# Performance work log

Measured on AMD Instinct MI355X. Metric: run time of the kernel, lower is better.

Reference implementation:

```python
import jax, jax.numpy as jnp
import numpy as np

N = 50000        # total nodes (disjoint batch of graphs)
E = 800000       # total edges
F_IN = 8         # node feature dim
S = 6            # edge feature dim
H = 20           # ECC kernel-network hidden size (hidden_states)
N_OUT = 20       # ECC output channels (n_out=hidden_states)
G = 32           # GCN channels
D1 = 16          # first dense
N_GRAPHS = 512   # graphs in batch


def setup_inputs() -> dict:
    key = jax.random.key(0)
    ks = jax.random.split(key, 24)
    r = lambda k, sh, s: jax.random.normal(k, sh, dtype=jnp.float32) * s
    return {
        "x": r(ks[0], (N, F_IN), 1.0),
        "e": r(ks[1], (E, S), 1.0),
        "edge_index": jax.random.randint(ks[2], (2, E), 0, N, dtype=jnp.int32),
        "seg": jnp.sort(jax.random.randint(ks[3], (N,), 0, N_GRAPHS, dtype=jnp.int32)),
        # ECC kernel network: S -> H -> H -> F_IN*N_OUT
        "ecc_w1": r(ks[4], (S, H), 0.4), "ecc_b1": jnp.zeros((H,), jnp.float32),
        "ecc_w2": r(ks[5], (H, H), 0.2), "ecc_b2": jnp.zeros((H,), jnp.float32),
        "ecc_w3": r(ks[6], (H, F_IN * N_OUT), 0.2), "ecc_b3": jnp.zeros((F_IN * N_OUT,), jnp.float32),
        "ecc_root": r(ks[7], (F_IN, N_OUT), 0.3), "ecc_b": jnp.zeros((N_OUT,), jnp.float32),
        "gcn1_w": r(ks[8], (N_OUT, G), 0.2), "gcn1_b": jnp.zeros((G,), jnp.float32),
        "gcn2_w": r(ks[9], (G, G), 0.2), "gcn2_b": jnp.zeros((G,), jnp.float32),
        "d1_w": r(ks[10], (G, D1), 0.2), "d1_b": jnp.zeros((D1,), jnp.float32),
        "d2_w": r(ks[11], (D1, 1), 0.2), "d2_b": jnp.zeros((1,), jnp.float32),
    }


def reference(x, e, edge_index, seg,
              ecc_w1, ecc_b1, ecc_w2, ecc_b2, ecc_w3, ecc_b3, ecc_root, ecc_b,
              gcn1_w, gcn1_b, gcn2_w, gcn2_b, d1_w, d1_b, d2_w, d2_b):
    row, col = edge_index[0], edge_index[1]  # message col -> row

    # --- ECCConv: per-edge MLP produces an [F_IN, N_OUT] filter per edge ---
    h = jax.nn.relu(e @ ecc_w1 + ecc_b1)
    h = jax.nn.relu(h @ ecc_w2 + ecc_b2)
    w_edge = (h @ ecc_w3 + ecc_b3).reshape(E, F_IN, N_OUT)   # [E, F_in, F_out]
    msg = jnp.einsum('ef,efo->eo', x[col], w_edge)            # per-edge message
    agg = jax.ops.segment_sum(msg, row, num_segments=N)
    x1 = jax.nn.relu(agg + x @ ecc_root + ecc_b)              # root + bias + relu

    # --- GCN normalization from the edge list (A + I, symmetric norm) ---
    deg = jax.ops.segment_sum(jnp.ones((E,), x.dtype), row, num_segments=N) + 1.0
    dinv = jax.lax.rsqrt(deg)
    edge_norm = (dinv[row] * dinv[col])[:, None]
    self_norm = (dinv * dinv)[:, None]

    def gcn(hin, W, b):
        hw = hin @ W
        nmsg = jax.ops.segment_sum(edge_norm * hw[col], row, num_segments=N)
        return jax.nn.relu(nmsg + self_norm * hw + b)

    x2 = gcn(x1, gcn1_w, gcn1_b)
    x3 = gcn(x2, gcn2_w, gcn2_b)

    # --- GlobalSumPool over graph ids, then MLP head ---
    pooled = jax.ops.segment_sum(x3, seg, num_segments=N_GRAPHS)  # [n_graphs, G]
    out = (pooled @ d1_w + d1_b) @ d2_w + d2_b                    # [n_graphs, 1]
    return out
```

## Files before the change

### kernel.cpp

```cpp
#include <hip/hip_runtime.h>
#include <hip/hip_bf16.h>

#define S_DIM   6
#define H_DIM   20
#define F_INN   8
#define N_OUTC  20
#define G_DIM   32
#define D1_DIM  16
#define NGRAPH  512
#define CAP     32

typedef short short8 __attribute__((ext_vector_type(8)));
typedef float floatx4 __attribute__((ext_vector_type(4)));

__device__ __forceinline__ unsigned short f2bf(float f) {
    unsigned u = __float_as_uint(f);
    return (unsigned short)((u + 0x8000u) >> 16);
}
__device__ __forceinline__ float bf2f(unsigned short s) {
    return __uint_as_float(((unsigned)s) << 16);
}
__device__ __forceinline__ unsigned pk2bf(float a, float b) {
    union { __hip_bfloat162 b2; unsigned u; } cv;
    cv.b2 = __float22bfloat162_rn(make_float2(a, b));
    return cv.u;
}

__global__ __launch_bounds__(256) void loc_kernel(
    const int* __restrict__ ei, int E, int* __restrict__ cnt,
    int* __restrict__ loc,
    const float* __restrict__ w3, const float* __restrict__ b3,
    unsigned short* __restrict__ B3f)
{
    int i = blockIdx.x * 256 + threadIdx.x;
    if (i < 6144) {
        int jj   = i & 7;
        int n    = (i >> 3) & 15;
        int quad = (i >> 7) & 3;
        int nt   = (i >> 9) & 1;
        int s    = i >> 10;
        int K = 32 * s + quad * 8 + jj;
        int o = n + 16 * nt;
        float v = 0.0f;
        if (o < N_OUTC) {
            if (K < 160)      v = w3[(K >> 3) * 160 + (K & 7) * N_OUTC + o];
            else if (K < 168) v = b3[(K - 160) * N_OUTC + o];
        }
        B3f[i] = f2bf(v);
    }
    if (i >= E) return;
    loc[i] = atomicAdd(&cnt[ei[i]], 1);
}

__global__ __launch_bounds__(256) void scanA_kernel(
    const int* __restrict__ deg, int N, int* __restrict__ bsum)
{
    int i = blockIdx.x * 256 + threadIdx.x;
    int v = (i < N) ? deg[i] : 0;
#pragma unroll
    for (int d = 1; d < 64; d <<= 1) v += __shfl_down(v, d, 64);
    __shared__ int ws[4];
    int wid = threadIdx.x >> 6;
    if ((threadIdx.x & 63) == 0) ws[wid] = v;
    __syncthreads();
    if (threadIdx.x == 0) bsum[blockIdx.x] = ws[0] + ws[1] + ws[2] + ws[3];
}

__global__ __launch_bounds__(256) void scanC_kernel(
    const int* __restrict__ deg, int N, const int* __restrict__ bsum, int nbl,
    int E, int* __restrict__ rowptr, float* __restrict__ dinv)
{
    __shared__ int ws[4];
    __shared__ int sboff;
    int t = threadIdx.x;
    {
        int v = (t < nbl && t < blockIdx.x) ? bsum[t] : 0;
#pragma unroll
        for (int d = 1; d < 64; d <<= 1) v += __shfl_down(v, d, 64);
        int wid = t >> 6;
        if ((t & 63) == 0) ws[wid] = v;
        __syncthreads();
        if (t == 0) sboff = ws[0] + ws[1] + ws[2] + ws[3];
        __syncthreads();
    }

    int i = blockIdx.x * 256 + t;
    int d0 = (i < N) ? deg[i] : 0;
    int v = d0;
#pragma unroll
    for (int d = 1; d < 64; d <<= 1) {
        int u = __shfl_up(v, d, 64);
        if ((t & 63) >= d) v += u;
    }
    __shared__ int ws2[4];
    int wid = t >> 6;
    if ((t & 63) == 63) ws2[wid] = v;
    __syncthreads();
    int woff = 0;
    for (int w = 0; w < wid; ++w) woff += ws2[w];
    if (i < N) {
        rowptr[i] = sboff + woff + v - d0;
        dinv[i] = rsqrtf((float)d0 + 1.0f);
    }
    if (blockIdx.x == 0 && t == 0) rowptr[N] = E;
}

__global__ __launch_bounds__(256) void build_kernel(
    const int* __restrict__ ei, int E, const float* __restrict__ e,
    const int* __restrict__ rowptr, const int* __restrict__ loc,
    const float* __restrict__ w1, const float* __restrict__ b1,
    const float* __restrict__ w2, const float* __restrict__ b2,
    int4* __restrict__ e_sorted)
{
    int i = blockIdx.x * 256 + threadIdx.x;
    if (i >= E) return;
    int r = ei[i];
    int c = ei[E + i];
    int p = rowptr[r] + loc[i];

    const float2* ep = (const float2*)&e[(size_t)i * S_DIM];
    float2 e0 = ep[0], e1 = ep[1], e2 = ep[2];
    float ef[S_DIM] = {e0.x, e0.y, e1.x, e1.y, e2.x, e2.y};

    float h1[H_DIM];
#pragma unroll
    for (int jj = 0; jj < H_DIM; ++jj) {
        float a = b1[jj];
#pragma unroll
        for (int s = 0; s < S_DIM; ++s) a = fmaf(ef[s], w1[s * H_DIM + jj], a);
        h1[jj] = fmaxf(a, 0.0f);
    }

    float h2[H_DIM];
#pragma unroll
    for (int jj = 0; jj < H_DIM; ++jj) {
        float a = b2[jj];
#pragma unroll
        for (int k = 0; k < H_DIM; ++k) a = fmaf(h1[k], w2[k * H_DIM + jj], a);
        h2[jj] = fmaxf(a, 0.0f);
    }

    int4 r0, r1, r2;
    r0.x = c;
    r0.y = (int)pk2bf(h2[0],  h2[1]);
    r0.z = (int)pk2bf(h2[2],  h2[3]);
    r0.w = (int)pk2bf(h2[4],  h2[5]);
    r1.x = (int)pk2bf(h2[6],  h2[7]);
    r1.y = (int)pk2bf(h2[8],  h2[9]);
    r1.z = (int)pk2bf(h2[10], h2[11]);
    r1.w = (int)pk2bf(h2[12], h2[13]);
    r2.x = (int)pk2bf(h2[14], h2[15]);
    r2.y = (int)pk2bf(h2[16], h2[17]);
    r2.z = (int)pk2bf(h2[18], h2[19]);
    r2.w = 0;

    int4* dst = &e_sorted[(size_t)p * 3];
    dst[0] = r0;
    dst[1] = r1;
    dst[2] = r2;
}

__global__ __launch_bounds__(256) void ecc_mfma_kernel(
    const int4* __restrict__ e_sorted, const float* __restrict__ x,
    const int* __restrict__ rowptr, int N, int E,
    const unsigned short* __restrict__ B3f,
    const float* __restrict__ root, const float* __restrict__ eb,
    const float* __restrict__ g1w,
    float* __restrict__ agg, int* __restrict__ col_sorted,
    unsigned short* __restrict__ hws1)
{
    __shared__ char smem[20480];
    __shared__ float x1buf[CAP * N_OUTC];
    __shared__ int rbounds[2];
    unsigned short (*h2b)[N_OUTC] = (unsigned short (*)[N_OUTC])smem;
    unsigned short (*xb)[F_INN]   = (unsigned short (*)[F_INN])(smem + 10240);
    float* lmsg = (float*)smem;

    int t = threadIdx.x;
    int j0 = blockIdx.x * 256;
    int jend = min(j0 + 256, E);
    int j = j0 + t;

    if (t < 2) {
        int s = (t == 0) ? j0 : (jend - 1);
        int lo = 0, hi = N - 1;
        while (lo < hi) {
            int m = (lo + hi + 1) >> 1;
            if (rowptr[m] <= s) lo = m; else hi = m - 1;
        }
        rbounds[t] = lo;
    }

    if (j < E) {
        const int4* er = &e_sorted[(size_t)j * 3];
        int4 r0 = er[0];
        int4 r1 = er[1];
        int4 r2 = er[2];
        int c = r0.x;
        col_sorted[j] = c;

        uint2* hdst = (uint2*)&h2b[t][0];
        hdst[0] = make_uint2((unsigned)r0.y, (unsigned)r0.z);
        hdst[1] = make_uint2((unsigned)r0.w, (unsigned)r1.x);
        hdst[2] = make_uint2((unsigned)r1.y, (unsigned)r1.z);
        hdst[3] = make_uint2((unsigned)r1.w, (unsigned)r2.x);
        hdst[4] = make_uint2((unsigned)r2.y, (unsigned)r2.z);

        const float4* xp = (const float4*)&x[(size_t)c * F_INN];
        float4 xa = xp[0], xb4 = xp[1];
        float xf[F_INN] = {xa.x, xa.y, xa.z, xa.w, xb4.x, xb4.y, xb4.z, xb4.w};
#pragma unroll
        for (int p = 0; p < F_INN / 2; ++p)
            *(unsigned*)&xb[t][2 * p] = pk2bf(xf[2 * p], xf[2 * p + 1]);
    } else {
        uint2* hdst = (uint2*)&h2b[t][0];
#pragma unroll
        for (int p = 0; p < 5; ++p) hdst[p] = make_uint2(0u, 0u);
#pragma unroll
        for (int p = 0; p < F_INN / 2; ++p) *(unsigned*)&xb[t][2 * p] = 0u;
    }
    __syncthreads();

    int lane = t & 63;
    int quad = lane >> 4;
    int n = lane & 15;
    const short8* Bg = (const short8*)B3f;
    short8 Bf[12];
#pragma unroll
    for (int s = 0; s < 6; ++s)
#pragma unroll
        for (int nt = 0; nt < 2; ++nt)
            Bf[s * 2 + nt] = Bg[((s * 2 + nt) * 4 + quad) * 16 + n];

    int w = t >> 6;
    floatx4 acc0s[4], acc1s[4];
#pragma unroll
    for (int T = 0; T < 4; ++T) {
        int base = w * 64 + T * 16;
        int m = base + n;

        const short8 xv8 = *(const short8*)&xb[m][0];
        float xfl[F_INN];
#pragma unroll
        for (int jj = 0; jj < F_INN; ++jj) xfl[jj] = bf2f((unsigned short)xv8[jj]);

        floatx4 acc0 = {0.f, 0.f, 0.f, 0.f};
        floatx4 acc1 = {0.f, 0.f, 0.f, 0.f};
#pragma unroll
        for (int s = 0; s < 6; ++s) {
            short8 A = {0, 0, 0, 0, 0, 0, 0, 0};
            if (s < 5) {
                float h = bf2f(h2b[m][4 * s + quad]);
                union { short8 s8; unsigned u[4]; } av;
#pragma unroll
                for (int p = 0; p < 4; ++p)
                    av.u[p] = pk2bf(h * xfl[2 * p], h * xfl[2 * p + 1]);
                A = av.s8;
            } else if (quad == 0) {
                A = xv8;
            }
            acc0 = __builtin_amdgcn_mfma_f32_16x16x32_bf16(A, Bf[s * 2 + 0], acc0, 0, 0, 0);
            acc1 = __builtin_amdgcn_mfma_f32_16x16x32_bf16(A, Bf[s * 2 + 1], acc1, 0, 0, 0);
        }
        acc0s[T] = acc0;
        acc1s[T] = acc1;
    }
    __syncthreads();

#pragma unroll
    for (int T = 0; T < 4; ++T) {
        int base = w * 64 + T * 16;
#pragma unroll
        for (int r = 0; r < 4; ++r) {
            int row = base + quad * 4 + r;
            lmsg[row * N_OUTC + n] = acc0s[T][r];
            if (n < 4) lmsg[row * N_OUTC + 16 + n] = acc1s[T][r];
        }
    }
    __syncthreads();

    int r0_ = rbounds[0], r1_ = rbounds[1];
    int nrows = r1_ - r0_ + 1;
    int work = nrows * 5;
    for (int ww = t; ww < work; ww += 256) {
        int idx = ww / 5;
        int q = ww - idx * 5;
        int row = r0_ + idx;
        int a0 = rowptr[row], a1 = rowptr[row + 1];
        int s0 = max(a0, j0), s1 = min(a1, jend);
        float ac0 = 0.f, ac1 = 0.f, ac2 = 0.f, ac3 = 0.f;
        for (int s = s0; s < s1; ++s) {
            const float4 v = *(const float4*)&lmsg[(s - j0) * N_OUTC + q * 4];
            ac0 += v.x; ac1 += v.y; ac2 += v.z; ac3 += v.w;
        }
        bool owned = (a0 >= j0 && a1 <= jend);
        if (owned && idx < CAP) {
            const float4* xp = (const float4*)&x[(size_t)row * F_INN];
            float4 xa = xp[0], xb4 = xp[1];
            float rx[F_INN] = {xa.x, xa.y, xa.z, xa.w, xb4.x, xb4.y, xb4.z, xb4.w};
            float av[4] = {ac0, ac1, ac2, ac3};
#pragma unroll
            for (int u = 0; u < 4; ++u) {
                int oc = q * 4 + u;
                float a = av[u] + eb[oc];
#pragma unroll
                for (int f = 0; f < F_INN; ++f)
                    a = fmaf(rx[f], root[f * N_OUTC + oc], a);
                x1buf[idx * N_OUTC + oc] = fmaxf(a, 0.0f);
            }
        } else {
            float* dst = &agg[(size_t)row * N_OUTC + q * 4];
            if (owned) {
                *(float4*)dst = make_float4(ac0, ac1, ac2, ac3);
            } else {
                unsafeAtomicAdd(dst + 0, ac0);
                unsafeAtomicAdd(dst + 1, ac1);
                unsafeAtomicAdd(dst + 2, ac2);
                unsafeAtomicAdd(dst + 3, ac3);
            }
        }
    }
    __syncthreads();

    int fast = min(nrows, CAP);
    int work2 = fast * 8;
    for (int ww = t; ww < work2; ww += 256) {
        int idx = ww >> 3;
        int qc = ww & 7;
        int row = r0_ + idx;
        int a0 = rowptr[row], a1 = rowptr[row + 1];
        if (!(a0 >= j0 && a1 <= jend)) continue;
        float di = rsqrtf((float)(a1 - a0) + 1.0f);
        float m0 = 0.f, m1 = 0.f, m2 = 0.f, m3 = 0.f;
        const float* xr = &x1buf[idx * N_OUTC];
#pragma unroll
        for (int o = 0; o < N_OUTC; ++o) {
            float xv = xr[o];
            const float4 g = *(const float4*)&g1w[o * G_DIM + qc * 4];
            m0 = fmaf(xv, g.x, m0); m1 = fmaf(xv, g.y, m1);
            m2 = fmaf(xv, g.z, m2); m3 = fmaf(xv, g.w, m3);
        }
        unsigned lo32 = pk2bf(m0 * di, m1 * di);
        unsigned hi32 = pk2bf(m2 * di, m3 * di);
        *(uint2*)&hws1[(size_t)row * G_DIM + qc * 4] = make_uint2(lo32, hi32);
    }
}

__global__ __launch_bounds__(256) void cleanup_kernel(
    const float* __restrict__ agg, const float* __restrict__ x,
    const int* __restrict__ rowptr, int N,
    const float* __restrict__ root, const float* __restrict__ eb,
    const float* __restrict__ g1w,
    unsigned short* __restrict__ hws1)
{
    int n = blockIdx.x * 256 + threadIdx.x;
    if (n >= N) return;
    int a0 = rowptr[n], a1 = rowptr[n + 1];
    bool contained = (a1 > a0) ? ((a0 >> 8) == ((a1 - 1) >> 8))
                               : ((a0 & 255) != 0);
    if (contained) {
        int target = (a0 >> 8) << 8;
        int lo = 0, hi = N - 1;
        while (lo < hi) {
            int m = (lo + hi + 1) >> 1;
            if (rowptr[m] <= target) lo = m; else hi = m - 1;
        }
        if (n - lo < CAP) return;
    }

    const float4* xp = (const float4*)&x[(size_t)n * F_INN];
    float4 xa = xp[0], xb = xp[1];
    float xf[F_INN] = {xa.x, xa.y, xa.z, xa.w, xb.x, xb.y, xb.z, xb.w};

    float x1[N_OUTC];
#pragma unroll
    for (int o = 0; o < N_OUTC; ++o) {
        float a = agg[(size_t)n * N_OUTC + o] + eb[o];
#pragma unroll
        for (int f = 0; f < F_INN; ++f) a = fmaf(xf[f], root[f * N_OUTC + o], a);
        x1[o] = fmaxf(a, 0.0f);
    }

    float di = rsqrtf((float)(a1 - a0) + 1.0f);
#pragma unroll
    for (int q = 0; q < 4; ++q) {
        float a[8];
#pragma unroll
        for (int u = 0; u < 8; ++u) {
            int g = q * 8 + u;
            float acc = 0.0f;
#pragma unroll
            for (int o = 0; o < N_OUTC; ++o) acc = fmaf(x1[o], g1w[o * G_DIM + g], acc);
            a[u] = acc * di;
        }
        union { short8 s8; unsigned u4[4]; } ov;
#pragma unroll
        for (int p = 0; p < 4; ++p) ov.u4[p] = pk2bf(a[2 * p], a[2 * p + 1]);
        *(short8*)&hws1[(size_t)n * G_DIM + q * 8] = ov.s8;
    }
}

template<bool DO_MATMUL>
__global__ __launch_bounds__(256) void gcn_gather_kernel(
    const unsigned short* __restrict__ hws, const int* __restrict__ rowptr,
    const int* __restrict__ col_sorted, const float* __restrict__ dinv, int N,
    const float* __restrict__ bias, const float* __restrict__ w2,
    unsigned short* __restrict__ outbuf)
{
    __shared__ float x2s[DO_MATMUL ? 32 * 33 : 1];
    __shared__ float w2s[DO_MATMUL ? G_DIM * G_DIM : 1];

    int t = threadIdx.x;
    int nl = t >> 3;
    int q = t & 7;
    int n = blockIdx.x * 32 + nl;

    if (DO_MATMUL) {
        ((float4*)w2s)[t] = ((const float4*)w2)[t];
        __syncthreads();
    }

    float xo[4];
    float di = 0.0f;
    if (n < N) {
        di = dinv[n];
        int j0 = rowptr[n], j1 = rowptr[n + 1];
        uint2 sv = *(const uint2*)&hws[(size_t)n * G_DIM + q * 4];
        float s[4];
        s[0] = bf2f((unsigned short)(sv.x & 0xffff));
        s[1] = bf2f((unsigned short)(sv.x >> 16));
        s[2] = bf2f((unsigned short)(sv.y & 0xffff));
        s[3] = bf2f((unsigned short)(sv.y >> 16));
        int j = j0;
        for (; j + 4 <= j1; j += 4) {
            int c0 = col_sorted[j + 0];
            int c1 = col_sorted[j + 1];
            int c2 = col_sorted[j + 2];
            int c3 = col_sorted[j + 3];
            uint2 v0 = *(const uint2*)&hws[(size_t)c0 * G_DIM + q * 4];
            uint2 v1 = *(const uint2*)&hws[(size_t)c1 * G_DIM + q * 4];
            uint2 v2 = *(const uint2*)&hws[(size_t)c2 * G_DIM + q * 4];
            uint2 v3 = *(const uint2*)&hws[(size_t)c3 * G_DIM + q * 4];
            s[0] += (bf2f((unsigned short)(v0.x & 0xffff)) + bf2f((unsigned short)(v1.x & 0xffff)))
                  + (bf2f((unsigned short)(v2.x & 0xffff)) + bf2f((unsigned short)(v3.x & 0xffff)));
            s[1] += (bf2f((unsigned short)(v0.x >> 16)) + bf2f((unsigned short)(v1.x >> 16)))
                  + (bf2f((unsigned short)(v2.x >> 16)) + bf2f((unsigned short)(v3.x >> 16)));
            s[2] += (bf2f((unsigned short)(v0.y & 0xffff)) + bf2f((unsigned short)(v1.y & 0xffff)))
                  + (bf2f((unsigned short)(v2.y & 0xffff)) + bf2f((unsigned short)(v3.y & 0xffff)));
            s[3] += (bf2f((unsigned short)(v0.y >> 16)) + bf2f((unsigned short)(v1.y >> 16)))
                  + (bf2f((unsigned short)(v2.y >> 16)) + bf2f((unsigned short)(v3.y >> 16)));
        }
        for (; j < j1; ++j) {
            int c = col_sorted[j];
            uint2 v = *(const uint2*)&hws[(size_t)c * G_DIM + q * 4];
            s[0] += bf2f((unsigned short)(v.x & 0xffff));
            s[1] += bf2f((unsigned short)(v.x >> 16));
            s[2] += bf2f((unsigned short)(v.y & 0xffff));
            s[3] += bf2f((unsigned short)(v.y >> 16));
        }
#pragma unroll
        for (int k = 0; k < 4; ++k)
            xo[k] = fmaxf(fmaf(di, s[k], bias[q * 4 + k]), 0.0f);
    } else {
#pragma unroll
        for (int k = 0; k < 4; ++k) xo[k] = 0.0f;
    }

    if (DO_MATMUL) {
#pragma unroll
        for (int k = 0; k < 4; ++k) x2s[nl * 33 + q * 4 + k] = xo[k];
        __syncthreads();
        if (n < N) {
            float a[4] = {0.f, 0.f, 0.f, 0.f};
#pragma unroll
            for (int g = 0; g < G_DIM; ++g) {
                float xv = x2s[nl * 33 + g];
#pragma unroll
                for (int k = 0; k < 4; ++k)
                    a[k] = fmaf(xv, w2s[g * G_DIM + q * 4 + k], a[k]);
            }
            uint2 ov = make_uint2(pk2bf(a[0] * di, a[1] * di),
                                  pk2bf(a[2] * di, a[3] * di));
            *(uint2*)&outbuf[(size_t)n * G_DIM + q * 4] = ov;
        }
    } else {
        if (n < N) {
            uint2 ov = make_uint2(pk2bf(xo[0], xo[1]), pk2bf(xo[2], xo[3]));
            *(uint2*)&outbuf[(size_t)n * G_DIM + q * 4] = ov;
        }
    }
}

__global__ __launch_bounds__(256) void pool_head_kernel(
    const unsigned short* __restrict__ x3, const int* __restrict__ seg, int N,
    const float* __restrict__ d1w, const float* __restrict__ d1b,
    const float* __restrict__ d2w, const float* __restrict__ d2b,
    float* __restrict__ out)
{
    __shared__ float red[8][G_DIM];
    __shared__ float pvec[G_DIM];
    __shared__ int bounds[2];
    int g = blockIdx.x;
    int t = threadIdx.x;
    if (t < 2) {
        int target = g + t;
        int lo = 0, hi = N;
        while (lo < hi) {
            int m = (lo + hi) >> 1;
            if (seg[m] < target) lo = m + 1; else hi = m;
        }
        bounds[t] = lo;
    }
    __syncthreads();
    int n0 = bounds[0], n1 = bounds[1];
    int ch = t & (G_DIM - 1);
    int slice = t >> 5;
    float a = 0.0f;
    for (int n = n0 + slice; n < n1; n += 8)
        a += bf2f(x3[(size_t)n * G_DIM + ch]);
    red[slice][ch] = a;
    __syncthreads();
    if (slice == 0) {
        float s = red[0][ch];
#pragma unroll
        for (int k = 1; k < 8; ++k) s += red[k][ch];
        pvec[ch] = s;
    }
    __syncthreads();
    if (t < 64) {
        float acc = 0.0f;
        if (t < D1_DIM) {
            float tj = d1b[t];
#pragma unroll
            for (int gg = 0; gg < G_DIM; ++gg)
                tj = fmaf(pvec[gg], d1w[gg * D1_DIM + t], tj);
            acc = tj * d2w[t];
        }
#pragma unroll
        for (int d = 1; d < D1_DIM; d <<= 1) acc += __shfl_down(acc, d, 64);
        if (t == 0) out[g] = acc + d2b[0];
    }
}

extern "C" void kernel_launch(void* const* d_in, const int* in_sizes, int n_in,
                              void* d_out, int out_size, void* d_ws, size_t ws_size,
                              hipStream_t stream)
{
    const float* x    = (const float*)d_in[0];
    const float* e    = (const float*)d_in[1];
    const int*   ei   = (const int*)d_in[2];
    const int*   seg  = (const int*)d_in[3];
    const float* w1   = (const float*)d_in[4];
    const float* b1   = (const float*)d_in[5];
    const float* w2   = (const float*)d_in[6];
    const float* b2   = (const float*)d_in[7];
    const float* w3   = (const float*)d_in[8];
    const float* b3   = (const float*)d_in[9];
    const float* root = (const float*)d_in[10];
    const float* eb   = (const float*)d_in[11];
    const float* g1w  = (const float*)d_in[12];
    const float* g1b  = (const float*)d_in[13];
    const float* g2w  = (const float*)d_in[14];
    const float* g2b  = (const float*)d_in[15];
    const float* d1w  = (const float*)d_in[16];
    const float* d1b  = (const float*)d_in[17];
    const float* d2w  = (const float*)d_in[18];
    const float* d2b  = (const float*)d_in[19];

    const int N = in_sizes[3];
    const int E = in_sizes[1] / S_DIM;
    float* out = (float*)d_out;

    const int nbl = (N + 255) / 256;
    const int ebl = (E + 255) / 256;

    char* ws = (char*)d_ws;
    size_t off = 0;
    auto alloc = [&](size_t elems) -> char* {
        char* p = ws + off;
        off += ((elems * 4 + 15) & ~(size_t)15);
        return p;
    };
    int*   cnt        = (int*)  alloc(N);
    float* agg        = (float*)alloc((size_t)N * N_OUTC);
    size_t zero_bytes = off;
    int*   rowptr     = (int*)  alloc(N + 1);
    int*   bsum       = (int*)  alloc(nbl);
    float* dinv       = (float*)alloc(N);
    int*   loc        = (int*)  alloc(E);
    int*   col_sorted = (int*)  alloc(E);
    unsigned short* B3f = (unsigned short*)alloc(6144 / 2);
    int4*  e_sorted   = (int4*) alloc((size_t)E * 12);
    unsigned short* hws1 = (unsigned short*)alloc((size_t)N * G_DIM / 2);
    unsigned short* hws2 = (unsigned short*)alloc((size_t)N * G_DIM / 2);
    unsigned short* x3   = (unsigned short*)alloc((size_t)N * G_DIM / 2);
    (void)ws_size;

    hipMemsetAsync(d_ws, 0, zero_bytes, stream);

    loc_kernel<<<ebl, 256, 0, stream>>>(ei, E, cnt, loc, w3, b3, B3f);
    scanA_kernel<<<nbl, 256, 0, stream>>>(cnt, N, bsum);
    scanC_kernel<<<nbl, 256, 0, stream>>>(cnt, N, bsum, nbl, E, rowptr, dinv);
    build_kernel<<<ebl, 256, 0, stream>>>(ei, E, e, rowptr, loc,
                                          w1, b1, w2, b2, e_sorted);
    ecc_mfma_kernel<<<ebl, 256, 0, stream>>>(e_sorted, x, rowptr, N, E, B3f,
                                             root, eb, g1w,
                                             agg, col_sorted, hws1);
    cleanup_kernel<<<nbl, 256, 0, stream>>>(agg, x, rowptr, N, root, eb, g1w, hws1);
    gcn_gather_kernel<true><<<(N + 31) / 32, 256, 0, stream>>>(
        hws1, rowptr, col_sorted, dinv, N, g1b, g2w, hws2);
    gcn_gather_kernel<false><<<(N + 31) / 32, 256, 0, stream>>>(
        hws2, rowptr, col_sorted, dinv, N, g2b, nullptr, x3);
    pool_head_kernel<<<NGRAPH, 256, 0, stream>>>(x3, seg, N, d1w, d1b, d2w, d2b, out);
}
```

Measured before the change: 273.8 us.

## Defer edge MLP layers into ECC kernel and store compact bf16 edge features

The build kernel now scatters only the column index and the six raw edge features (packed as bf16) into a 16-byte sorted record, instead of running the first two kernel-network layers and storing 20 bf16 hidden values in 48 bytes. The two small MLP layers are recomputed in the ECC MFMA kernel right after loading the record. This cuts the scatter write and the subsequent read of the intermediate buffer to a third. In exchange, the ECC kernel carries more register and ALU work, and raw edge features are rounded to bf16 before the first layer, which adds precision loss.

```diff
diff --git a/kernel.cpp b/kernel.cpp
--- a/kernel.cpp
+++ b/kernel.cpp
@@ -108,8 +108,6 @@
 __global__ __launch_bounds__(256) void build_kernel(
     const int* __restrict__ ei, int E, const float* __restrict__ e,
     const int* __restrict__ rowptr, const int* __restrict__ loc,
-    const float* __restrict__ w1, const float* __restrict__ b1,
-    const float* __restrict__ w2, const float* __restrict__ b2,
     int4* __restrict__ e_sorted)
 {
     int i = blockIdx.x * 256 + threadIdx.x;
@@ -120,50 +118,21 @@
 
     const float2* ep = (const float2*)&e[(size_t)i * S_DIM];
     float2 e0 = ep[0], e1 = ep[1], e2 = ep[2];
-    float ef[S_DIM] = {e0.x, e0.y, e1.x, e1.y, e2.x, e2.y};
-
-    float h1[H_DIM];
-#pragma unroll
-    for (int jj = 0; jj < H_DIM; ++jj) {
-        float a = b1[jj];
-#pragma unroll
-        for (int s = 0; s < S_DIM; ++s) a = fmaf(ef[s], w1[s * H_DIM + jj], a);
-        h1[jj] = fmaxf(a, 0.0f);
-    }
-
-    float h2[H_DIM];
-#pragma unroll
-    for (int jj = 0; jj < H_DIM; ++jj) {
-        float a = b2[jj];
-#pragma unroll
-        for (int k = 0; k < H_DIM; ++k) a = fmaf(h1[k], w2[k * H_DIM + jj], a);
-        h2[jj] = fmaxf(a, 0.0f);
-    }
-
-    int4 r0, r1, r2;
-    r0.x = c;
-    r0.y = (int)pk2bf(h2[0],  h2[1]);
-    r0.z = (int)pk2bf(h2[2],  h2[3]);
-    r0.w = (int)pk2bf(h2[4],  h2[5]);
-    r1.x = (int)pk2bf(h2[6],  h2[7]);
-    r1.y = (int)pk2bf(h2[8],  h2[9]);
-    r1.z = (int)pk2bf(h2[10], h2[11]);
-    r1.w = (int)pk2bf(h2[12], h2[13]);
-    r2.x = (int)pk2bf(h2[14], h2[15]);
-    r2.y = (int)pk2bf(h2[16], h2[17]);
-    r2.z = (int)pk2bf(h2[18], h2[19]);
-    r2.w = 0;
-
-    int4* dst = &e_sorted[(size_t)p * 3];
-    dst[0] = r0;
-    dst[1] = r1;
-    dst[2] = r2;
+
+    int4 rec;
+    rec.x = c;
+    rec.y = (int)pk2bf(e0.x, e0.y);
+    rec.z = (int)pk2bf(e1.x, e1.y);
+    rec.w = (int)pk2bf(e2.x, e2.y);
+    e_sorted[p] = rec;
 }
 
 __global__ __launch_bounds__(256) void ecc_mfma_kernel(
     const int4* __restrict__ e_sorted, const float* __restrict__ x,
     const int* __restrict__ rowptr, int N, int E,
     const unsigned short* __restrict__ B3f,
+    const float* __restrict__ w1, const float* __restrict__ b1,
+    const float* __restrict__ w2, const float* __restrict__ b2,
     const float* __restrict__ root, const float* __restrict__ eb,
     const float* __restrict__ g1w,
     float* __restrict__ agg, int* __restrict__ col_sorted,
@@ -192,32 +161,51 @@
     }
 
     if (j < E) {
-        const int4* er = &e_sorted[(size_t)j * 3];
-        int4 r0 = er[0];
-        int4 r1 = er[1];
-        int4 r2 = er[2];
-        int c = r0.x;
+        int4 rec = e_sorted[j];
+        int c = rec.x;
         col_sorted[j] = c;
-
-        uint2* hdst = (uint2*)&h2b[t][0];
-        hdst[0] = make_uint2((unsigned)r0.y, (unsigned)r0.z);
-        hdst[1] = make_uint2((unsigned)r0.w, (unsigned)r1.x);
-        hdst[2] = make_uint2((unsigned)r1.y, (unsigned)r1.z);
-        hdst[3] = make_uint2((unsigned)r1.w, (unsigned)r2.x);
-        hdst[4] = make_uint2((unsigned)r2.y, (unsigned)r2.z);
+        float ef[S_DIM] = {
+            bf2f((unsigned short)(rec.y & 0xffff)),
+            bf2f((unsigned short)((unsigned)rec.y >> 16)),
+            bf2f((unsigned short)(rec.z & 0xffff)),
+            bf2f((unsigned short)((unsigned)rec.z >> 16)),
+            bf2f((unsigned short)(rec.w & 0xffff)),
+            bf2f((unsigned short)((unsigned)rec.w >> 16))
+        };
+
+        float h1[H_DIM];
+#pragma unroll
+        for (int jj = 0; jj < H_DIM; ++jj) {
+            float a = b1[jj];
+#pragma unroll
+            for (int s = 0; s < S_DIM; ++s) a = fmaf(ef[s], w1[s * H_DIM + jj], a);
+            h1[jj] = fmaxf(a, 0.0f);
+        }
+
+        float h2[H_DIM];
+#pragma unroll
+        for (int jj = 0; jj < H_DIM; ++jj) {
+            float a = b2[jj];
+#pragma unroll
+            for (int k = 0; k < H_DIM; ++k) a = fmaf(h1[k], w2[k * H_DIM + jj], a);
+            h2[jj] = fmaxf(a, 0.0f);
+        }
 
         const float4* xp = (const float4*)&x[(size_t)c * F_INN];
         float4 xa = xp[0], xb4 = xp[1];
         float xf[F_INN] = {xa.x, xa.y, xa.z, xa.w, xb4.x, xb4.y, xb4.z, xb4.w};
+
+#pragma unroll
+        for (int p = 0; p < N_OUTC / 2; ++p)
+            *(unsigned*)&h2b[t][2 * p] = pk2bf(h2[2 * p], h2[2 * p + 1]);
 #pragma unroll
         for (int p = 0; p < F_INN / 2; ++p)
             *(unsigned*)&xb[t][2 * p] = pk2bf(xf[2 * p], xf[2 * p + 1]);
     } else {
-        uint2* hdst = (uint2*)&h2b[t][0];
-#pragma unroll
-        for (int p = 0; p < 5; ++p) hdst[p] = make_uint2(0u, 0u);
-#pragma unroll
-        for (int p = 0; p < F_INN / 2; ++p) *(unsigned*)&xb[t][2 * p] = 0u;
+#pragma unroll
+        for (int p = 0; p < N_OUTC / 2; ++p) *(unsigned*)&h2b[t][2 * p] = 0u;
+#pragma unroll
+        for (int p = 0; p < F_INN / 2; ++p)  *(unsigned*)&xb[t][2 * p] = 0u;
     }
     __syncthreads();
 
@@ -279,13 +267,13 @@
     }
     __syncthreads();
 
-    int r0_ = rbounds[0], r1_ = rbounds[1];
-    int nrows = r1_ - r0_ + 1;
+    int r0 = rbounds[0], r1 = rbounds[1];
+    int nrows = r1 - r0 + 1;
     int work = nrows * 5;
     for (int ww = t; ww < work; ww += 256) {
         int idx = ww / 5;
         int q = ww - idx * 5;
-        int row = r0_ + idx;
+        int row = r0 + idx;
         int a0 = rowptr[row], a1 = rowptr[row + 1];
         int s0 = max(a0, j0), s1 = min(a1, jend);
         float ac0 = 0.f, ac1 = 0.f, ac2 = 0.f, ac3 = 0.f;
@@ -327,7 +315,7 @@
     for (int ww = t; ww < work2; ww += 256) {
         int idx = ww >> 3;
         int qc = ww & 7;
-        int row = r0_ + idx;
+        int row = r0 + idx;
         int a0 = rowptr[row], a1 = rowptr[row + 1];
         if (!(a0 >= j0 && a1 <= jend)) continue;
         float di = rsqrtf((float)(a1 - a0) + 1.0f);
@@ -590,7 +578,7 @@
     int*   loc        = (int*)  alloc(E);
     int*   col_sorted = (int*)  alloc(E);
     unsigned short* B3f = (unsigned short*)alloc(6144 / 2);
-    int4*  e_sorted   = (int4*) alloc((size_t)E * 12);
+    int4*  e_sorted   = (int4*) alloc((size_t)E * 4);
     unsigned short* hws1 = (unsigned short*)alloc((size_t)N * G_DIM / 2);
     unsigned short* hws2 = (unsigned short*)alloc((size_t)N * G_DIM / 2);
     unsigned short* x3   = (unsigned short*)alloc((size_t)N * G_DIM / 2);
@@ -601,10 +589,9 @@
     loc_kernel<<<ebl, 256, 0, stream>>>(ei, E, cnt, loc, w3, b3, B3f);
     scanA_kernel<<<nbl, 256, 0, stream>>>(cnt, N, bsum);
     scanC_kernel<<<nbl, 256, 0, stream>>>(cnt, N, bsum, nbl, E, rowptr, dinv);
-    build_kernel<<<ebl, 256, 0, stream>>>(ei, E, e, rowptr, loc,
-                                          w1, b1, w2, b2, e_sorted);
+    build_kernel<<<ebl, 256, 0, stream>>>(ei, E, e, rowptr, loc, e_sorted);
     ecc_mfma_kernel<<<ebl, 256, 0, stream>>>(e_sorted, x, rowptr, N, E, B3f,
-                                             root, eb, g1w,
+                                             w1, b1, w2, b2, root, eb, g1w,
                                              agg, col_sorted, hws1);
     cleanup_kernel<<<nbl, 256, 0, stream>>>(agg, x, rowptr, N, root, eb, g1w, hws1);
     gcn_gather_kernel<true><<<(N + 31) / 32, 256, 0, stream>>>(
```

New measurement: 266.7 us. 2.6% less time.
